# Performance work log

Measured on AMD Instinct MI355X. Metric: run time of the kernel, lower is better.

The kernel has to match this reference:

```python
import jax, jax.numpy as jnp
import numpy as np

N = 100000   # nodes
DEG = 4      # fixed out-degree (>2 so every node survives the c>2 mask)
E = N * DEG  # edges
IN = 128
H = 256


def _lin_params(key, fan_out, fan_in, bias=True):
    k1, k2 = jax.random.split(key)
    W = 0.05 * jax.random.normal(k1, (fan_out, fan_in), jnp.float32)
    if bias:
        b = 0.05 * jax.random.normal(k2, (fan_out,), jnp.float32)
        return W, b
    return W


def setup_inputs() -> dict:
    key = jax.random.key(0)
    ks = jax.random.split(key, 12)
    x = jax.random.normal(ks[0], (N, IN), jnp.float32)
    # every node has exactly DEG outgoing edges -> out-degree 4 > 2 for all nodes
    src = jnp.repeat(jnp.arange(N, dtype=jnp.int32), DEG)
    dst = jax.random.randint(ks[1], (E,), 0, N, dtype=jnp.int32)
    edge_index = jnp.stack([src, dst])  # [2, E]
    batch = jnp.zeros((N,), jnp.int32)
    Wr0, br0 = _lin_params(ks[2], H, IN)
    Ws0 = _lin_params(ks[3], H, IN, bias=False)
    Wr1, br1 = _lin_params(ks[4], H, H)
    Ws1 = _lin_params(ks[5], H, H, bias=False)
    Wr2, br2 = _lin_params(ks[6], H, H)
    Ws2 = _lin_params(ks[7], H, H, bias=False)
    Wsp1, bsp1 = _lin_params(ks[8], 1, H)
    Wsp2, bsp2 = _lin_params(ks[9], 1, H)
    Wl, bl = _lin_params(ks[10], 1, 2)
    return dict(x=x, edge_index=edge_index, batch=batch,
                Wr0=Wr0, br0=br0, Ws0=Ws0,
                Wr1=Wr1, br1=br1, Ws1=Ws1,
                Wr2=Wr2, br2=br2, Ws2=Ws2,
                Wsp1=Wsp1, bsp1=bsp1, Wsp2=Wsp2, bsp2=bsp2,
                Wl=Wl, bl=bl)


def reference(x, edge_index, batch, Wr0, br0, Ws0, Wr1, br1, Ws1,
              Wr2, br2, Ws2, Wsp1, bsp1, Wsp2, bsp2, Wl, bl):
    src, dst = edge_index[0], edge_index[1]

    def gconv(h, Wr, br, Ws):
        # PyG GraphConv(aggr='add'): out_i = W_rel @ sum_{j->i} h_j + b + W_root @ h_i
        agg = jax.ops.segment_sum(h[src], dst, num_segments=N)
        return jax.nn.relu(agg @ Wr.T + br + h @ Ws.T)

    h = gconv(x, Wr0, br0, Ws0)
    h = gconv(h, Wr1, br1, Ws1)
    h = gconv(h, Wr2, br2, Ws2)

    # unique(edge_index[0], counts) ; keep source nodes with out-degree > 2
    deg = jax.ops.segment_sum(jnp.ones((E,), h.dtype), src, num_segments=N)
    sel = jnp.nonzero(deg > 2, size=N, fill_value=0)[0]  # all N nodes by construction
    xs = h[sel].reshape(-1, 2 * H)  # pair consecutive nodes
    x1, x2 = xs[:, :H], xs[:, H:]
    out = jnp.concatenate([jax.nn.relu(x1 @ Wsp1.T + bsp1),
                           jax.nn.relu(x2 @ Wsp2.T + bsp2)], axis=1)
    y = jax.nn.sigmoid(out @ Wl.T + bl)  # split=True branch
    return y, xs, x1, x2
```

## Files before the change

kernel.cpp:

```cpp
#include <hip/hip_runtime.h>
#include <hip/hip_bf16.h>
#include <math.h>

#define NNODES 100000
#define NEDGES 400000
#define INDIM  128
#define HDIM   256
#define MAXDEG 32

#define BM 128
#define BN 128
#define BK 64

typedef __attribute__((ext_vector_type(8))) short short8;
typedef __attribute__((ext_vector_type(4))) float f32x4;

__device__ __forceinline__ float bf2f(unsigned short u) {
    union { unsigned int i; float f; } v; v.i = ((unsigned int)u) << 16; return v.f;
}
__device__ __forceinline__ unsigned short f2bf(float f) {
    union { float f; unsigned int i; } v; v.f = f;
    unsigned int r = v.i + 0x7fffu + ((v.i >> 16) & 1u);
    return (unsigned short)(r >> 16);
}

__device__ __forceinline__ void async_load16(const void* g, void* l) {
    __builtin_amdgcn_global_load_lds(
        (const __attribute__((address_space(1))) unsigned int*)g,
        (__attribute__((address_space(3))) unsigned int*)l,
        16, 0, 0);
}

__global__ void build_elist(const int* __restrict__ ei, int* __restrict__ cnt,
                            int* __restrict__ elist) {
    int e = blockIdx.x * 256 + threadIdx.x;
    if (e < NEDGES) {
        int d = ei[NEDGES + e];
        int s = ei[e];
        int pos = atomicAdd(&cnt[d], 1);
        if (pos < MAXDEG) elist[d * MAXDEG + pos] = s;
    }
}

__global__ void convert_x(const float* __restrict__ x, unsigned short* __restrict__ xb) {
    int i = blockIdx.x * 256 + threadIdx.x;
    const int total = NNODES * INDIM / 4;
    if (i < total) {
        float4 v = ((const float4*)x)[i];
        ushort4 o; o.x = f2bf(v.x); o.y = f2bf(v.y); o.z = f2bf(v.z); o.w = f2bf(v.w);
        ((ushort4*)xb)[i] = o;
    }
}

__global__ void convert_w(const float* __restrict__ Wr, const float* __restrict__ Ws,
                          unsigned short* __restrict__ B, int K) {
    int idx = blockIdx.x * 256 + threadIdx.x;
    int tot = HDIM * 2 * K;
    if (idx < tot) {
        int n = idx / (2 * K);
        int k = idx - n * 2 * K;
        float v = (k < K) ? Wr[n * K + k] : Ws[n * K + (k - K)];
        B[idx] = f2bf(v);
    }
}

__global__ void gather_f32(const float* __restrict__ x, const int* __restrict__ cnt,
                           const int* __restrict__ elist, unsigned short* __restrict__ agg) {
    int wid  = (blockIdx.x * blockDim.x + threadIdx.x) >> 6;
    int lane = threadIdx.x & 63;
    if (wid >= NNODES) return;
    int c = cnt[wid]; if (c > MAXDEG) c = MAXDEG;
    const int* el = elist + wid * MAXDEG;
    float a0 = 0.f, a1 = 0.f;
    for (int j = 0; j < c; j++) {
        int s = el[j];
        float2 v = ((const float2*)(x + (size_t)s * INDIM))[lane];
        a0 += v.x; a1 += v.y;
    }
    ushort2 o; o.x = f2bf(a0); o.y = f2bf(a1);
    ((ushort2*)(agg + (size_t)wid * INDIM))[lane] = o;
}

__global__ void gather_bf16(const unsigned short* __restrict__ h, const int* __restrict__ cnt,
                            const int* __restrict__ elist, unsigned short* __restrict__ agg) {
    int wid  = (blockIdx.x * blockDim.x + threadIdx.x) >> 6;
    int lane = threadIdx.x & 63;
    if (wid >= NNODES) return;
    int c = cnt[wid]; if (c > MAXDEG) c = MAXDEG;
    const int* el = elist + wid * MAXDEG;
    float a0 = 0.f, a1 = 0.f, a2 = 0.f, a3 = 0.f;
    for (int j = 0; j < c; j++) {
        int s = el[j];
        ushort4 v = ((const ushort4*)(h + (size_t)s * HDIM))[lane];
        a0 += bf2f(v.x); a1 += bf2f(v.y); a2 += bf2f(v.z); a3 += bf2f(v.w);
    }
    ushort4 o; o.x = f2bf(a0); o.y = f2bf(a1); o.z = f2bf(a2); o.w = f2bf(a3);
    ((ushort4*)(agg + (size_t)wid * HDIM))[lane] = o;
}

template<int MODE>
__global__ __launch_bounds__(256)
void gemm_kernel(const unsigned short* __restrict__ A1, const unsigned short* __restrict__ A2,
                 int K, const unsigned short* __restrict__ B, const float* __restrict__ bias,
                 unsigned short* __restrict__ hout,
                 float* __restrict__ xs, float* __restrict__ x1o, float* __restrict__ x2o) {
    __shared__ unsigned short Ash[BM * BK];
    __shared__ unsigned short Bsh[BN * BK];

    const int tid  = threadIdx.x;
    const int lane = tid & 63;
    const int wave = tid >> 6;
    const int wm = wave >> 1, wn = wave & 1;
    const int m0 = blockIdx.x * BM;
    const int n0 = blockIdx.y * BN;
    const int Ktot = 2 * K;

    f32x4 acc[4][4];
    for (int i = 0; i < 4; i++)
        for (int j = 0; j < 4; j++)
            acc[i][j] = (f32x4){0.f, 0.f, 0.f, 0.f};

    for (int k0 = 0; k0 < Ktot; k0 += BK) {
        const unsigned short* Abase; int koff;
        if (k0 < K) { Abase = A1; koff = k0; } else { Abase = A2; koff = k0 - K; }

        #pragma unroll
        for (int it = 0; it < 4; it++) {
            int idx = it * 256 + tid;
            int row = idx >> 3, seg = idx & 7;
            int gseg = seg ^ (row & 7);
            int grow = m0 + row; if (grow >= NNODES) grow = NNODES - 1;
            async_load16(Abase + (size_t)grow * K + koff + gseg * 8, &Ash[idx * 8]);
        }
        #pragma unroll
        for (int it = 0; it < 4; it++) {
            int idx = it * 256 + tid;
            int row = idx >> 3, seg = idx & 7;
            int gseg = seg ^ (row & 7);
            int grow = n0 + row;
            async_load16(B + (size_t)grow * Ktot + k0 + gseg * 8, &Bsh[idx * 8]);
        }
        __syncthreads();

        #pragma unroll
        for (int half = 0; half < 2; half++) {
            short8 af[4], bfr[4];
            #pragma unroll
            for (int mt = 0; mt < 4; mt++) {
                int ml  = wm * 64 + mt * 16 + (lane & 15);
                int seg = half * 4 + (lane >> 4);
                int ps  = seg ^ (ml & 7);
                af[mt] = *(const short8*)&Ash[ml * BK + ps * 8];
            }
            #pragma unroll
            for (int nt = 0; nt < 4; nt++) {
                int nl  = wn * 64 + nt * 16 + (lane & 15);
                int seg = half * 4 + (lane >> 4);
                int ps  = seg ^ (nl & 7);
                bfr[nt] = *(const short8*)&Bsh[nl * BK + ps * 8];
            }
            #pragma unroll
            for (int mt = 0; mt < 4; mt++)
                #pragma unroll
                for (int nt = 0; nt < 4; nt++)
                    acc[mt][nt] = __builtin_amdgcn_mfma_f32_16x16x32_bf16(
                        af[mt], bfr[nt], acc[mt][nt], 0, 0, 0);
        }
        __syncthreads();
    }

    #pragma unroll
    for (int mt = 0; mt < 4; mt++) {
        int rbase = m0 + wm * 64 + mt * 16 + (lane >> 4) * 4;
        #pragma unroll
        for (int nt = 0; nt < 4; nt++) {
            int gc = n0 + wn * 64 + nt * 16 + (lane & 15);
            float bv = bias[gc];
            #pragma unroll
            for (int r = 0; r < 4; r++) {
                int grow = rbase + r;
                if (grow >= NNODES) continue;
                float v = acc[mt][nt][r] + bv;
                v = v > 0.f ? v : 0.f;
                if (MODE == 0) {
                    hout[(size_t)grow * HDIM + gc] = f2bf(v);
                } else {
                    xs[(size_t)grow * HDIM + gc] = v;
                    int pr = grow >> 1;
                    if (grow & 1) x2o[(size_t)pr * HDIM + gc] = v;
                    else          x1o[(size_t)pr * HDIM + gc] = v;
                }
            }
        }
    }
}

__global__ void head_kernel(const float* __restrict__ h3, const float* __restrict__ Wsp1,
                            const float* __restrict__ bsp1, const float* __restrict__ Wsp2,
                            const float* __restrict__ bsp2, const float* __restrict__ Wl,
                            const float* __restrict__ bl, float* __restrict__ y) {
    int wid  = (blockIdx.x * blockDim.x + threadIdx.x) >> 6;
    int lane = threadIdx.x & 63;
    if (wid >= NNODES / 2) return;
    float4 a  = ((const float4*)(h3 + (size_t)(2 * wid) * HDIM))[lane];
    float4 w1 = ((const float4*)Wsp1)[lane];
    float4 c  = ((const float4*)(h3 + (size_t)(2 * wid + 1) * HDIM))[lane];
    float4 w2 = ((const float4*)Wsp2)[lane];
    float s1 = a.x * w1.x + a.y * w1.y + a.z * w1.z + a.w * w1.w;
    float s2 = c.x * w2.x + c.y * w2.y + c.z * w2.z + c.w * w2.w;
    #pragma unroll
    for (int off = 32; off; off >>= 1) {
        s1 += __shfl_down(s1, off);
        s2 += __shfl_down(s2, off);
    }
    if (lane == 0) {
        s1 += bsp1[0]; s2 += bsp2[0];
        s1 = s1 > 0.f ? s1 : 0.f;
        s2 = s2 > 0.f ? s2 : 0.f;
        float t = s1 * Wl[0] + s2 * Wl[1] + bl[0];
        y[wid] = 1.f / (1.f + expf(-t));
    }
}

extern "C" void kernel_launch(void* const* d_in, const int* in_sizes, int n_in,
                              void* d_out, int out_size, void* d_ws, size_t ws_size,
                              hipStream_t stream) {
    const float* x    = (const float*)d_in[0];
    const int*   ei   = (const int*)d_in[1];
    const float* Wr0  = (const float*)d_in[3];
    const float* br0  = (const float*)d_in[4];
    const float* Ws0  = (const float*)d_in[5];
    const float* Wr1  = (const float*)d_in[6];
    const float* br1  = (const float*)d_in[7];
    const float* Ws1  = (const float*)d_in[8];
    const float* Wr2  = (const float*)d_in[9];
    const float* br2  = (const float*)d_in[10];
    const float* Ws2  = (const float*)d_in[11];
    const float* Wsp1 = (const float*)d_in[12];
    const float* bsp1 = (const float*)d_in[13];
    const float* Wsp2 = (const float*)d_in[14];
    const float* bsp2 = (const float*)d_in[15];
    const float* Wl   = (const float*)d_in[16];
    const float* bl   = (const float*)d_in[17];

    char* ws = (char*)d_ws;
    size_t off = 0;
    auto alloc = [&](size_t bytes) -> void* {
        void* p = ws + off;
        off += (bytes + 255) & ~(size_t)255;
        return p;
    };
    int*            cnt   = (int*)alloc((size_t)NNODES * 4);
    int*            elist = (int*)alloc((size_t)NNODES * MAXDEG * 4);
    unsigned short* xb    = (unsigned short*)alloc((size_t)NNODES * INDIM * 2);
    unsigned short* aggb  = (unsigned short*)alloc((size_t)NNODES * HDIM * 2);
    unsigned short* hA    = (unsigned short*)alloc((size_t)NNODES * HDIM * 2);
    unsigned short* hB    = (unsigned short*)alloc((size_t)NNODES * HDIM * 2);
    unsigned short* B0    = (unsigned short*)alloc((size_t)HDIM * 2 * INDIM * 2);
    unsigned short* B1    = (unsigned short*)alloc((size_t)HDIM * 2 * HDIM * 2);
    unsigned short* B2    = (unsigned short*)alloc((size_t)HDIM * 2 * HDIM * 2);

    float* y  = (float*)d_out;
    float* xs = y + 50000;
    float* x1 = xs + (size_t)50000 * 512;
    float* x2 = x1 + (size_t)50000 * 256;

    hipMemsetAsync(cnt, 0, (size_t)NNODES * 4, stream);
    build_elist<<<(NEDGES + 255) / 256, 256, 0, stream>>>(ei, cnt, elist);
    convert_x<<<(NNODES * INDIM / 4 + 255) / 256, 256, 0, stream>>>(x, xb);
    convert_w<<<(HDIM * 2 * INDIM + 255) / 256, 256, 0, stream>>>(Wr0, Ws0, B0, INDIM);
    convert_w<<<(HDIM * 2 * HDIM + 255) / 256, 256, 0, stream>>>(Wr1, Ws1, B1, HDIM);
    convert_w<<<(HDIM * 2 * HDIM + 255) / 256, 256, 0, stream>>>(Wr2, Ws2, B2, HDIM);

    dim3 gg((NNODES + BM - 1) / BM, HDIM / BN);
    int gather_blocks = (NNODES * 64 + 255) / 256;

    gather_f32<<<gather_blocks, 256, 0, stream>>>(x, cnt, elist, aggb);
    gemm_kernel<0><<<gg, 256, 0, stream>>>(aggb, xb, INDIM, B0, br0, hA, nullptr, nullptr, nullptr);
    gather_bf16<<<gather_blocks, 256, 0, stream>>>(hA, cnt, elist, aggb);
    gemm_kernel<0><<<gg, 256, 0, stream>>>(aggb, hA, HDIM, B1, br1, hB, nullptr, nullptr, nullptr);
    gather_bf16<<<gather_blocks, 256, 0, stream>>>(hB, cnt, elist, aggb);
    gemm_kernel<1><<<gg, 256, 0, stream>>>(aggb, hB, HDIM, B2, br2, nullptr, xs, x1, x2);
    head_kernel<<<((NNODES / 2) * 64 + 255) / 256, 256, 0, stream>>>(
        xs, Wsp1, bsp1, Wsp2, bsp2, Wl, bl, y);
}
```

Before: 652.0 us.

## Fuse split-head dot products into final GEMM epilogue and vectorize stores via LDS

```diff
diff --git a/kernel.cpp b/kernel.cpp
--- a/kernel.cpp
+++ b/kernel.cpp
@@ -11,8 +11,11 @@
 #define BM 128
 #define BN 128
 #define BK 64
+#define MTILES 782
+#define GEMM_BLOCKS 1568
 
 typedef __attribute__((ext_vector_type(8))) short short8;
+typedef __attribute__((ext_vector_type(8))) unsigned short ushort8v;
 typedef __attribute__((ext_vector_type(4))) float f32x4;
 
 __device__ __forceinline__ float bf2f(unsigned short u) {
@@ -70,12 +73,18 @@
     int lane = threadIdx.x & 63;
     if (wid >= NNODES) return;
     int c = cnt[wid]; if (c > MAXDEG) c = MAXDEG;
-    const int* el = elist + wid * MAXDEG;
+    const int4* el4 = (const int4*)(elist + wid * MAXDEG);
     float a0 = 0.f, a1 = 0.f;
-    for (int j = 0; j < c; j++) {
-        int s = el[j];
-        float2 v = ((const float2*)(x + (size_t)s * INDIM))[lane];
-        a0 += v.x; a1 += v.y;
+    for (int j0 = 0; j0 < c; j0 += 4) {
+        int4 e = el4[j0 >> 2];
+        int rem = c - j0;
+        float2 v0 = {0.f,0.f}, v1 = {0.f,0.f}, v2 = {0.f,0.f}, v3 = {0.f,0.f};
+        v0 = ((const float2*)(x + (size_t)e.x * INDIM))[lane];
+        if (rem > 1) v1 = ((const float2*)(x + (size_t)e.y * INDIM))[lane];
+        if (rem > 2) v2 = ((const float2*)(x + (size_t)e.z * INDIM))[lane];
+        if (rem > 3) v3 = ((const float2*)(x + (size_t)e.w * INDIM))[lane];
+        a0 += v0.x + v1.x + v2.x + v3.x;
+        a1 += v0.y + v1.y + v2.y + v3.y;
     }
     ushort2 o; o.x = f2bf(a0); o.y = f2bf(a1);
     ((ushort2*)(agg + (size_t)wid * INDIM))[lane] = o;
@@ -87,12 +96,20 @@
     int lane = threadIdx.x & 63;
     if (wid >= NNODES) return;
     int c = cnt[wid]; if (c > MAXDEG) c = MAXDEG;
-    const int* el = elist + wid * MAXDEG;
+    const int4* el4 = (const int4*)(elist + wid * MAXDEG);
     float a0 = 0.f, a1 = 0.f, a2 = 0.f, a3 = 0.f;
-    for (int j = 0; j < c; j++) {
-        int s = el[j];
-        ushort4 v = ((const ushort4*)(h + (size_t)s * HDIM))[lane];
-        a0 += bf2f(v.x); a1 += bf2f(v.y); a2 += bf2f(v.z); a3 += bf2f(v.w);
+    for (int j0 = 0; j0 < c; j0 += 4) {
+        int4 e = el4[j0 >> 2];
+        int rem = c - j0;
+        ushort4 v0 = {0,0,0,0}, v1 = {0,0,0,0}, v2 = {0,0,0,0}, v3 = {0,0,0,0};
+        v0 = ((const ushort4*)(h + (size_t)e.x * HDIM))[lane];
+        if (rem > 1) v1 = ((const ushort4*)(h + (size_t)e.y * HDIM))[lane];
+        if (rem > 2) v2 = ((const ushort4*)(h + (size_t)e.z * HDIM))[lane];
+        if (rem > 3) v3 = ((const ushort4*)(h + (size_t)e.w * HDIM))[lane];
+        a0 += bf2f(v0.x) + bf2f(v1.x) + bf2f(v2.x) + bf2f(v3.x);
+        a1 += bf2f(v0.y) + bf2f(v1.y) + bf2f(v2.y) + bf2f(v3.y);
+        a2 += bf2f(v0.z) + bf2f(v1.z) + bf2f(v2.z) + bf2f(v3.z);
+        a3 += bf2f(v0.w) + bf2f(v1.w) + bf2f(v2.w) + bf2f(v3.w);
     }
     ushort4 o; o.x = f2bf(a0); o.y = f2bf(a1); o.z = f2bf(a2); o.w = f2bf(a3);
     ((ushort4*)(agg + (size_t)wid * HDIM))[lane] = o;
@@ -103,16 +120,25 @@
 void gemm_kernel(const unsigned short* __restrict__ A1, const unsigned short* __restrict__ A2,
                  int K, const unsigned short* __restrict__ B, const float* __restrict__ bias,
                  unsigned short* __restrict__ hout,
-                 float* __restrict__ xs, float* __restrict__ x1o, float* __restrict__ x2o) {
-    __shared__ unsigned short Ash[BM * BK];
-    __shared__ unsigned short Bsh[BN * BK];
+                 float* __restrict__ xs, float* __restrict__ x1o, float* __restrict__ x2o,
+                 const float* __restrict__ Wsp1, const float* __restrict__ Wsp2,
+                 float* __restrict__ spart) {
+    __shared__ __align__(16) unsigned char smem[(BM * BK + BN * BK) * 2];
+    unsigned short* Ash = (unsigned short*)smem;
+    unsigned short* Bsh = Ash + BM * BK;
+
+    int u = blockIdx.x;
+    int g = u >> 4, r = u & 15;
+    int ny = (r >> 3) & 1;
+    int mx = g * 8 + (r & 7);
+    if (mx >= MTILES) return;
 
     const int tid  = threadIdx.x;
     const int lane = tid & 63;
     const int wave = tid >> 6;
     const int wm = wave >> 1, wn = wave & 1;
-    const int m0 = blockIdx.x * BM;
-    const int n0 = blockIdx.y * BN;
+    const int m0 = mx * BM;
+    const int n0 = ny * BN;
     const int Ktot = 2 * K;
 
     f32x4 acc[4][4];
@@ -169,56 +195,79 @@
         __syncthreads();
     }
 
+    float* bounce = (float*)smem;
+    float* wb = bounce + wave * (16 * 68);
+    const int q    = lane & 3;
+    const int rrow = lane >> 2;
+
     #pragma unroll
     for (int mt = 0; mt < 4; mt++) {
-        int rbase = m0 + wm * 64 + mt * 16 + (lane >> 4) * 4;
-        #pragma unroll
-        for (int nt = 0; nt < 4; nt++) {
-            int gc = n0 + wn * 64 + nt * 16 + (lane & 15);
-            float bv = bias[gc];
-            #pragma unroll
-            for (int r = 0; r < 4; r++) {
-                int grow = rbase + r;
-                if (grow >= NNODES) continue;
-                float v = acc[mt][nt][r] + bv;
-                v = v > 0.f ? v : 0.f;
-                if (MODE == 0) {
-                    hout[(size_t)grow * HDIM + gc] = f2bf(v);
-                } else {
-                    xs[(size_t)grow * HDIM + gc] = v;
-                    int pr = grow >> 1;
-                    if (grow & 1) x2o[(size_t)pr * HDIM + gc] = v;
-                    else          x1o[(size_t)pr * HDIM + gc] = v;
+        __syncthreads();
+        #pragma unroll
+        for (int nt = 0; nt < 4; nt++)
+            #pragma unroll
+            for (int rr = 0; rr < 4; rr++)
+                wb[((lane >> 4) * 4 + rr) * 68 + nt * 16 + (lane & 15)] = acc[mt][nt][rr];
+        __syncthreads();
+
+        int grow = m0 + wm * 64 + mt * 16 + rrow;
+        int gc   = n0 + wn * 64 + q * 16;
+        float4 v[4];
+        #pragma unroll
+        for (int s = 0; s < 4; s++)
+            v[s] = ((const float4*)(wb + rrow * 68 + q * 16))[s];
+
+        if (grow < NNODES) {
+            const float4* bv = (const float4*)(bias + gc);
+            #pragma unroll
+            for (int s = 0; s < 4; s++) {
+                float4 b4 = bv[s];
+                v[s].x = fmaxf(v[s].x + b4.x, 0.f);
+                v[s].y = fmaxf(v[s].y + b4.y, 0.f);
+                v[s].z = fmaxf(v[s].z + b4.z, 0.f);
+                v[s].w = fmaxf(v[s].w + b4.w, 0.f);
+            }
+            if (MODE == 0) {
+                ushort8v o0, o1;
+                o0[0]=f2bf(v[0].x); o0[1]=f2bf(v[0].y); o0[2]=f2bf(v[0].z); o0[3]=f2bf(v[0].w);
+                o0[4]=f2bf(v[1].x); o0[5]=f2bf(v[1].y); o0[6]=f2bf(v[1].z); o0[7]=f2bf(v[1].w);
+                o1[0]=f2bf(v[2].x); o1[1]=f2bf(v[2].y); o1[2]=f2bf(v[2].z); o1[3]=f2bf(v[2].w);
+                o1[4]=f2bf(v[3].x); o1[5]=f2bf(v[3].y); o1[6]=f2bf(v[3].z); o1[7]=f2bf(v[3].w);
+                ushort8v* dst = (ushort8v*)(hout + (size_t)grow * HDIM + gc);
+                dst[0] = o0; dst[1] = o1;
+            } else {
+                float4* xsp = (float4*)(xs + (size_t)grow * HDIM + gc);
+                #pragma unroll
+                for (int s = 0; s < 4; s++) xsp[s] = v[s];
+                float* xo = (grow & 1) ? x2o : x1o;
+                float4* xop = (float4*)(xo + (size_t)(grow >> 1) * HDIM + gc);
+                #pragma unroll
+                for (int s = 0; s < 4; s++) xop[s] = v[s];
+                const float* wsp = (grow & 1) ? Wsp2 : Wsp1;
+                const float4* wv = (const float4*)(wsp + gc);
+                float p = 0.f;
+                #pragma unroll
+                for (int s = 0; s < 4; s++) {
+                    float4 w4 = wv[s];
+                    p += v[s].x * w4.x + v[s].y * w4.y + v[s].z * w4.z + v[s].w * w4.w;
                 }
+                p += __shfl_xor(p, 1);
+                p += __shfl_xor(p, 2);
+                if (q == 0) atomicAdd(&spart[grow], p);
             }
         }
     }
 }
 
-__global__ void head_kernel(const float* __restrict__ h3, const float* __restrict__ Wsp1,
-                            const float* __restrict__ bsp1, const float* __restrict__ Wsp2,
-                            const float* __restrict__ bsp2, const float* __restrict__ Wl,
-                            const float* __restrict__ bl, float* __restrict__ y) {
-    int wid  = (blockIdx.x * blockDim.x + threadIdx.x) >> 6;
-    int lane = threadIdx.x & 63;
-    if (wid >= NNODES / 2) return;
-    float4 a  = ((const float4*)(h3 + (size_t)(2 * wid) * HDIM))[lane];
-    float4 w1 = ((const float4*)Wsp1)[lane];
-    float4 c  = ((const float4*)(h3 + (size_t)(2 * wid + 1) * HDIM))[lane];
-    float4 w2 = ((const float4*)Wsp2)[lane];
-    float s1 = a.x * w1.x + a.y * w1.y + a.z * w1.z + a.w * w1.w;
-    float s2 = c.x * w2.x + c.y * w2.y + c.z * w2.z + c.w * w2.w;
-    #pragma unroll
-    for (int off = 32; off; off >>= 1) {
-        s1 += __shfl_down(s1, off);
-        s2 += __shfl_down(s2, off);
-    }
-    if (lane == 0) {
-        s1 += bsp1[0]; s2 += bsp2[0];
-        s1 = s1 > 0.f ? s1 : 0.f;
-        s2 = s2 > 0.f ? s2 : 0.f;
+__global__ void finalize_kernel(const float* __restrict__ spart, const float* __restrict__ bsp1,
+                                const float* __restrict__ bsp2, const float* __restrict__ Wl,
+                                const float* __restrict__ bl, float* __restrict__ y) {
+    int p = blockIdx.x * 256 + threadIdx.x;
+    if (p < NNODES / 2) {
+        float s1 = spart[2 * p]     + bsp1[0]; s1 = s1 > 0.f ? s1 : 0.f;
+        float s2 = spart[2 * p + 1] + bsp2[0]; s2 = s2 > 0.f ? s2 : 0.f;
         float t = s1 * Wl[0] + s2 * Wl[1] + bl[0];
-        y[wid] = 1.f / (1.f + expf(-t));
+        y[p] = 1.f / (1.f + expf(-t));
     }
 }
 
@@ -251,6 +300,8 @@
         return p;
     };
     int*            cnt   = (int*)alloc((size_t)NNODES * 4);
+    float*          spart = (float*)alloc((size_t)NNODES * 4);
+    size_t zero_bytes = off;
     int*            elist = (int*)alloc((size_t)NNODES * MAXDEG * 4);
     unsigned short* xb    = (unsigned short*)alloc((size_t)NNODES * INDIM * 2);
     unsigned short* aggb  = (unsigned short*)alloc((size_t)NNODES * HDIM * 2);
@@ -265,22 +316,26 @@
     float* x1 = xs + (size_t)50000 * 512;
     float* x2 = x1 + (size_t)50000 * 256;
 
-    hipMemsetAsync(cnt, 0, (size_t)NNODES * 4, stream);
+    hipMemsetAsync(ws, 0, zero_bytes, stream);
     build_elist<<<(NEDGES + 255) / 256, 256, 0, stream>>>(ei, cnt, elist);
     convert_x<<<(NNODES * INDIM / 4 + 255) / 256, 256, 0, stream>>>(x, xb);
     convert_w<<<(HDIM * 2 * INDIM + 255) / 256, 256, 0, stream>>>(Wr0, Ws0, B0, INDIM);
     convert_w<<<(HDIM * 2 * HDIM + 255) / 256, 256, 0, stream>>>(Wr1, Ws1, B1, HDIM);
     convert_w<<<(HDIM * 2 * HDIM + 255) / 256, 256, 0, stream>>>(Wr2, Ws2, B2, HDIM);
 
-    dim3 gg((NNODES + BM - 1) / BM, HDIM / BN);
     int gather_blocks = (NNODES * 64 + 255) / 256;
 
     gather_f32<<<gather_blocks, 256, 0, stream>>>(x, cnt, elist, aggb);
-    gemm_kernel<0><<<gg, 256, 0, stream>>>(aggb, xb, INDIM, B0, br0, hA, nullptr, nullptr, nullptr);
+    gemm_kernel<0><<<GEMM_BLOCKS, 256, 0, stream>>>(aggb, xb, INDIM, B0, br0, hA,
+                                                    nullptr, nullptr, nullptr,
+                                                    nullptr, nullptr, nullptr);
     gather_bf16<<<gather_blocks, 256, 0, stream>>>(hA, cnt, elist, aggb);
-    gemm_kernel<0><<<gg, 256, 0, stream>>>(aggb, hA, HDIM, B1, br1, hB, nullptr, nullptr, nullptr);
+    gemm_kernel<0><<<GEMM_BLOCKS, 256, 0, stream>>>(aggb, hA, HDIM, B1, br1, hB,
+                                                    nullptr, nullptr, nullptr,
+                                                    nullptr, nullptr, nullptr);
     gather_bf16<<<gather_blocks, 256, 0, stream>>>(hB, cnt, elist, aggb);
-    gemm_kernel<1><<<gg, 256, 0, stream>>>(aggb, hB, HDIM, B2, br2, nullptr, xs, x1, x2);
-    head_kernel<<<((NNODES / 2) * 64 + 255) / 256, 256, 0, stream>>>(
-        xs, Wsp1, bsp1, Wsp2, bsp2, Wl, bl, y);
-}
+    gemm_kernel<1><<<GEMM_BLOCKS, 256, 0, stream>>>(aggb, hB, HDIM, B2, br2, nullptr,
+                                                    xs, x1, x2, Wsp1, Wsp2, spart);
+    finalize_kernel<<<(NNODES / 2 + 255) / 256, 256, 0, stream>>>(
+        spart, bsp1, bsp2, Wl, bl, y);
+}
```

New measurement: 618.3 us. 1.05x faster.
